# Performance work log

Hardware: AMD Instinct MI355X
Metric: run time of the kernel (lower is better)

## Reference

```python
import jax, jax.numpy as jnp
import numpy as np

# SLAYER SRM-alpha neuron constants (from network.yaml defaults)
THETA = 10.0      # spike threshold
TAU_S = 10.0      # PSP (srm) time constant
TAU_R = 1.0       # refractory time constant
TS = 1.0          # simulation timestep
TAU_RHO = 1.0     # surrogate gradient width
SCALE_RHO = 1.0   # surrogate gradient scale
E = float(np.e)

@jax.custom_vjp
def spike_fn(v):
    # Heaviside threshold; surrogate gradient in bwd (SLAYER spike pdf)
    return (v >= 0).astype(v.dtype)

def _spike_fwd(v):
    return spike_fn(v), v

def _spike_bwd(v, g):
    sg = (SCALE_RHO / TAU_RHO) * jnp.exp(-jnp.abs(v) / TAU_RHO)
    return (g * sg,)

spike_fn.defvjp(_spike_fwd, _spike_bwd)

def psp_spike(a):
    """SLAYER psp (alpha SRM kernel eps(t)=(t/tau_s)e^{1-t/tau_s}, IIR form)
    followed by spike generation with refractory feedback
    nu(t) = -2*theta*(t/tau_r)e^{1-t/tau_r}. a: [B,C,T] -> spikes [B,C,T].
    Alpha kernels realized exactly as 2-state linear recursions."""
    ds = jnp.exp(jnp.asarray(-TS / TAU_S, a.dtype))
    dr = jnp.exp(jnp.asarray(-TS / TAU_R, a.dtype))
    cs = E / TAU_S
    cr = -2.0 * THETA * E / TAU_R
    B, C, T = a.shape
    z = jnp.zeros((B, C), a.dtype)

    def step(carry, a_t):
        xs, ys, xr, yr = carry
        u = cs * ys + cr * yr          # membrane = psp(a) + refractory
        s = spike_fn(u - THETA)
        xs = ds * xs + a_t             # first-order stage (input)
        ys = ds * (ys + TS * xs)       # alpha stage: ys[t+1]=d*(ys+Ts*xs)
        xr = dr * xr + s               # refractory stages driven by spikes
        yr = dr * (yr + TS * xr)
        return (xs, ys, xr, yr), s

    _, s = jax.lax.scan(step, (z, z, z, z), jnp.moveaxis(a, -1, 0))
    return jnp.moveaxis(s, 0, -1)

def psp(a):
    """Pure SLAYER psp filter (no spiking). a: [B,C,T] -> [B,C,T]."""
    ds = jnp.exp(jnp.asarray(-TS / TAU_S, a.dtype))
    cs = E / TAU_S
    B, C, T = a.shape
    z = jnp.zeros((B, C), a.dtype)

    def step(carry, a_t):
        xs, ys = carry
        p = cs * ys
        xs = ds * xs + a_t
        ys = ds * (ys + TS * xs)
        return (xs, ys), p

    _, p = jax.lax.scan(step, (z, z), jnp.moveaxis(a, -1, 0))
    return jnp.moveaxis(p, 0, -1)

def setup_inputs() -> dict:
    key = jax.random.key(0)
    k1, k2, k3 = jax.random.split(key, 3)
    B, NIN, H, NOUT, T = 64, 4, 512, 2, 2000
    # sparse binary input spike trains, rate ~0.1
    spikeInput = (jax.random.uniform(k1, (B, NIN, T)) < 0.1).astype(jnp.float32)
    W1 = 2.0 * jax.random.normal(k2, (H, NIN), jnp.float32)
    W2 = 2.0 * jax.random.normal(k3, (NOUT, H), jnp.float32)
    return {"spikeInput": spikeInput, "W1": W1, "W2": W2}

def reference(spikeInput, W1, W2):
    # fc1 -> psp -> spike
    s1 = psp_spike(jnp.einsum('oi,bit->bot', W1, spikeInput))
    # fc2 -> psp -> spike
    s2 = psp_spike(jnp.einsum('oh,bht->bot', W2, s1))
    # final psp readout
    return psp(s2)
```

## Files before the change

kernel.cpp:

```cpp
#include <hip/hip_runtime.h>
#include <cstdint>
#include <cstddef>

#define THETA_F 10.0f
#define DS_C 0.9048374180359595731642491f
#define DR_C 0.3678794411714423215955238f
#define CS_C 0.2718281828459045235360287f
#define CR_C -54.3656365691809047072057f
#define P100_C 4.5399929762484854e-05f
#define QC100_C 4.1079555325e-03f

typedef unsigned int       u32;
typedef unsigned long long u64;
typedef unsigned short     u16;

#define W32_WORDS_PER_B  (62 * 512)
#define TAIL_BYTE_OFF    (64 * 62 * 512 * 4)

__global__ __launch_bounds__(128) void k1_layer1(
    const float* __restrict__ inp,
    const float* __restrict__ W1,
    u32* __restrict__ w32, u16* __restrict__ tail16)
{
    __shared__ float table[16 * 128];
    __shared__ alignas(8) unsigned char codes[2048];

    const int tid = threadIdx.x;
    const int b   = blockIdx.x >> 2;
    const int h   = ((blockIdx.x & 3) << 7) + tid;

    const float w0 = W1[h * 4 + 0];
    const float w1 = W1[h * 4 + 1];
    const float w2 = W1[h * 4 + 2];
    const float w3 = W1[h * 4 + 3];
    for (int c = 0; c < 16; ++c) {
        float v = __fmul_rn(w0, (c & 1) ? 1.0f : 0.0f);
        v = __fadd_rn(v, __fmul_rn(w1, (c & 2) ? 1.0f : 0.0f));
        v = __fadd_rn(v, __fmul_rn(w2, (c & 4) ? 1.0f : 0.0f));
        v = __fadd_rn(v, __fmul_rn(w3, (c & 8) ? 1.0f : 0.0f));
        table[c * 128 + tid] = v;
    }
    for (int t = tid; t < 2000; t += 128) {
        const float v0 = inp[(b * 4 + 0) * 2000 + t];
        const float v1 = inp[(b * 4 + 1) * 2000 + t];
        const float v2 = inp[(b * 4 + 2) * 2000 + t];
        const float v3 = inp[(b * 4 + 3) * 2000 + t];
        codes[t] = (unsigned char)((int)(v0 != 0.0f) | ((int)(v1 != 0.0f) << 1) |
                                   ((int)(v2 != 0.0f) << 2) | ((int)(v3 != 0.0f) << 3));
    }
    if (tid < 48) codes[2000 + tid] = 0;
    __syncthreads();

#define ISSUE(CW, BUF) do {                                                   \
        const u32 lo_ = (u32)(CW), hi_ = (u32)((CW) >> 32);                   \
        BUF[0] = table[((lo_      ) & 15) * 128 + tid];                       \
        BUF[1] = table[((lo_ >>  8) & 15) * 128 + tid];                       \
        BUF[2] = table[((lo_ >> 16) & 15) * 128 + tid];                       \
        BUF[3] = table[((lo_ >> 24) & 15) * 128 + tid];                       \
        BUF[4] = table[((hi_      ) & 15) * 128 + tid];                       \
        BUF[5] = table[((hi_ >>  8) & 15) * 128 + tid];                       \
        BUF[6] = table[((hi_ >> 16) & 15) * 128 + tid];                       \
        BUF[7] = table[((hi_ >> 24) & 15) * 128 + tid];                       \
    } while (0)

#define STEP(AV, BITPOS) do {                                                 \
        const float u_ = __fadd_rn(__fmul_rn(CS_C, ys), __fmul_rn(CR_C, yr)); \
        const bool sp_ = (u_ >= THETA_F);                                     \
        xs = __fadd_rn(__fmul_rn(DS_C, xs), (AV));                            \
        ys = __fmul_rn(DS_C, __fadd_rn(ys, xs));                              \
        const float A_ = __fmul_rn(DR_C, xr);                                 \
        xr = sp_ ? __fadd_rn(A_, 1.0f) : A_;                                  \
        yr = __fmul_rn(DR_C, __fadd_rn(yr, xr));                              \
        bits = sp_ ? (bits | (1u << (BITPOS))) : bits;                        \
    } while (0)

#define STEP8(BUF, J0) do {                                                   \
        _Pragma("unroll")                                                     \
        for (int j_ = 0; j_ < 8; ++j_) STEP(BUF[j_], (J0) + j_);              \
    } while (0)

    float xs = 0.0f, ys = 0.0f, xr = 0.0f, yr = 0.0f;
    u32 bits = 0;
    u32* pw = w32 + (size_t)b * W32_WORDS_PER_B + h;

    float bA[8], bB[8];
    u64 cw = *reinterpret_cast<const u64*>(codes);
    ISSUE(cw, bA);
    u64 c1 = *reinterpret_cast<const u64*>(codes + 8);
    u64 c2 = *reinterpret_cast<const u64*>(codes + 16);
    u64 c3 = *reinterpret_cast<const u64*>(codes + 24);
    u64 c4 = *reinterpret_cast<const u64*>(codes + 32);

    for (int t0 = 0; t0 < 1984; t0 += 32) {
        ISSUE(c1, bB);
        const u64 n1 = *reinterpret_cast<const u64*>(codes + t0 + 40);
        const u64 n2 = *reinterpret_cast<const u64*>(codes + t0 + 48);
        const u64 n3 = *reinterpret_cast<const u64*>(codes + t0 + 56);
        const u64 n4 = *reinterpret_cast<const u64*>(codes + t0 + 64);
        STEP8(bA, 0);
        ISSUE(c2, bA);
        STEP8(bB, 8);
        ISSUE(c3, bB);
        STEP8(bA, 16);
        ISSUE(c4, bA);
        STEP8(bB, 24);
        *pw = bits; pw += 512; bits = 0;
        c1 = n1; c2 = n2; c3 = n3; c4 = n4;
    }
    ISSUE(c1, bB);
    STEP8(bA, 0);
    STEP8(bB, 8);
    tail16[b * 512 + h] = (u16)bits;

#undef STEP8
#undef STEP
#undef ISSUE
}

__global__ __launch_bounds__(256) void k2_fc2(
    const u32* __restrict__ w32, const u16* __restrict__ tail16,
    const float* __restrict__ W2,
    float* __restrict__ a2)
{
    __shared__ float w2s[1024];
    __shared__ u32 stage[4096];

    const int tid = threadIdx.x;
    const int b  = blockIdx.x >> 3;
    const int it = blockIdx.x & 7;

    for (int j = tid; j < 1024; j += 256) w2s[j] = W2[j];
    #pragma unroll
    for (int k = 0; k < 16; ++k) {
        const int l = tid + (k << 8);
        const int gtb = (it << 3) + (l >> 9);
        u32 v = 0;
        if (gtb < 62)       v = w32[((size_t)b * 62 + gtb) * 512 + (l & 511)];
        else if (gtb == 62) v = (u32)tail16[b * 512 + (l & 511)];
        stage[l] = v;
    }
    __syncthreads();

    const int t = (it << 8) + tid;
    if (t < 2000) {
        const u32* srow = stage + ((tid >> 5) << 9);
        const int sh = tid & 31;
        float acc0 = 0.0f, acc1 = 0.0f;
        #pragma unroll 8
        for (int hh = 0; hh < 512; ++hh) {
            const bool on = (srow[hh] >> sh) & 1u;
            acc0 = __fadd_rn(acc0, on ? w2s[hh] : 0.0f);
            acc1 = __fadd_rn(acc1, on ? w2s[512 + hh] : 0.0f);
        }
        a2[(size_t)(b * 2 + 0) * 2000 + t] = acc0;
        a2[(size_t)(b * 2 + 1) * 2000 + t] = acc1;
    }
}

__global__ __launch_bounds__(80) void k3all(
    const float* __restrict__ a2, float* __restrict__ out)
{
    __shared__ float U[4][2000];
    __shared__ unsigned char s2b[4][2000];
    __shared__ float ex[4][20], ey[4][20], px[4][20], py[4][20];

    const int tid = threadIdx.x;
    const int lc  = tid / 20;
    const int ck  = tid - lc * 20;
    const int chain = blockIdx.x * 4 + lc;

    {
        const float* segi = a2 + (size_t)chain * 2000 + ck * 100;
        float* segU = &U[lc][ck * 100];
        float X = 0.0f, Y = 0.0f;
        for (int g = 0; g < 25; ++g) {
            float4 qv = *reinterpret_cast<const float4*>(segi + 4 * g);
            float z;
            z = __fmul_rn(CS_C, Y); X = __fmaf_rn(DS_C, X, qv.x);
            Y = __fmul_rn(DS_C, __fadd_rn(Y, X)); qv.x = z;
            z = __fmul_rn(CS_C, Y); X = __fmaf_rn(DS_C, X, qv.y);
            Y = __fmul_rn(DS_C, __fadd_rn(Y, X)); qv.y = z;
            z = __fmul_rn(CS_C, Y); X = __fmaf_rn(DS_C, X, qv.z);
            Y = __fmul_rn(DS_C, __fadd_rn(Y, X)); qv.z = z;
            z = __fmul_rn(CS_C, Y); X = __fmaf_rn(DS_C, X, qv.w);
            Y = __fmul_rn(DS_C, __fadd_rn(Y, X)); qv.w = z;
            *reinterpret_cast<float4*>(segU + 4 * g) = qv;
        }
        ex[lc][ck] = X; ey[lc][ck] = Y;
    }
    __syncthreads();
    if (tid < 4) {
        float x = 0.0f, y = 0.0f;
        for (int c = 0; c < 20; ++c) {
            px[tid][c] = x; py[tid][c] = y;
            const float xn = __fmaf_rn(P100_C, x, ex[tid][c]);
            const float yn = __fadd_rn(
                __fmaf_rn(QC100_C, x, __fmul_rn(P100_C, y)), ey[tid][c]);
            x = xn; y = yn;
        }
    }
    __syncthreads();
    {
        float xh = px[lc][ck], yh = py[lc][ck];
        float* segU = &U[lc][ck * 100];
        if (ck != 0) {
            for (int g = 0; g < 25; ++g) {
                float4 qv = *reinterpret_cast<const float4*>(segU + 4 * g);
                qv.x = __fmaf_rn(CS_C, yh, qv.x);
                xh = __fmul_rn(DS_C, xh); yh = __fmul_rn(DS_C, __fadd_rn(yh, xh));
                qv.y = __fmaf_rn(CS_C, yh, qv.y);
                xh = __fmul_rn(DS_C, xh); yh = __fmul_rn(DS_C, __fadd_rn(yh, xh));
                qv.z = __fmaf_rn(CS_C, yh, qv.z);
                xh = __fmul_rn(DS_C, xh); yh = __fmul_rn(DS_C, __fadd_rn(yh, xh));
                qv.w = __fmaf_rn(CS_C, yh, qv.w);
                xh = __fmul_rn(DS_C, xh); yh = __fmul_rn(DS_C, __fadd_rn(yh, xh));
                *reinterpret_cast<float4*>(segU + 4 * g) = qv;
            }
        }
    }
    __syncthreads();

    {
        float xr2 = 0.0f, yr2 = 0.0f;
#define RSTEP(UV) do {                                                        \
        const float u_ = __fadd_rn((UV), __fmul_rn(CR_C, yr2));               \
        const bool sp_ = (u_ >= THETA_F);                                     \
        const float A_ = __fmul_rn(DR_C, xr2);                                \
        xr2 = sp_ ? __fadd_rn(A_, 1.0f) : A_;                                 \
        yr2 = __fmul_rn(DR_C, __fadd_rn(yr2, xr2));                           \
    } while (0)
        if (ck != 0) {
            const float* wseg = &U[lc][ck * 100 - 64];
            #pragma unroll
            for (int g = 0; g < 16; ++g) {
                const float4 qv = *reinterpret_cast<const float4*>(wseg + 4 * g);
                RSTEP(qv.x); RSTEP(qv.y); RSTEP(qv.z); RSTEP(qv.w);
            }
        }
        const float* eseg = &U[lc][ck * 100];
        unsigned char* ob = &s2b[lc][ck * 100];
        for (int g = 0; g < 25; ++g) {
            const float4 qv = *reinterpret_cast<const float4*>(eseg + 4 * g);
            const float uv[4] = {qv.x, qv.y, qv.z, qv.w};
            #pragma unroll
            for (int j = 0; j < 4; ++j) {
                const float u_ = __fadd_rn(uv[j], __fmul_rn(CR_C, yr2));
                const bool sp_ = (u_ >= THETA_F);
                ob[4 * g + j] = sp_ ? 1 : 0;
                const float A_ = __fmul_rn(DR_C, xr2);
                xr2 = sp_ ? __fadd_rn(A_, 1.0f) : A_;
                yr2 = __fmul_rn(DR_C, __fadd_rn(yr2, xr2));
            }
        }
#undef RSTEP
    }
    __syncthreads();

    float* sego = out + (size_t)chain * 2000 + ck * 100;
    {
        const unsigned char* si = &s2b[lc][ck * 100];
        float X = 0.0f, Y = 0.0f;
        for (int j = 0; j < 100; ++j) {
            const float a = (float)si[j];
            const float z = __fmul_rn(CS_C, Y);
            X = __fmaf_rn(DS_C, X, a);
            Y = __fmul_rn(DS_C, __fadd_rn(Y, X));
            sego[j] = z;
        }
        ex[lc][ck] = X; ey[lc][ck] = Y;
    }
    __syncthreads();
    if (tid < 4) {
        float x = 0.0f, y = 0.0f;
        for (int c = 0; c < 20; ++c) {
            px[tid][c] = x; py[tid][c] = y;
            const float xn = __fmaf_rn(P100_C, x, ex[tid][c]);
            const float yn = __fadd_rn(
                __fmaf_rn(QC100_C, x, __fmul_rn(P100_C, y)), ey[tid][c]);
            x = xn; y = yn;
        }
    }
    __syncthreads();
    {
        float xh = px[lc][ck], yh = py[lc][ck];
        if (ck != 0) {
            for (int j = 0; j < 100; ++j) {
                sego[j] = __fmaf_rn(CS_C, yh, sego[j]);
                xh = __fmul_rn(DS_C, xh);
                yh = __fmul_rn(DS_C, __fadd_rn(yh, xh));
            }
        }
    }
}

extern "C" void kernel_launch(void* const* d_in, const int* in_sizes, int n_in,
                              void* d_out, int out_size, void* d_ws, size_t ws_size,
                              hipStream_t stream)
{
    const float* inp = (const float*)d_in[0];
    const float* W1  = (const float*)d_in[1];
    const float* W2  = (const float*)d_in[2];
    float* out = (float*)d_out;

    u32* w32    = (u32*)d_ws;
    u16* tail16 = (u16*)((char*)d_ws + TAIL_BYTE_OFF);

    k1_layer1<<<dim3(256), dim3(128), 0, stream>>>(inp, W1, w32, tail16);
    k2_fc2<<<dim3(512), dim3(256), 0, stream>>>(w32, tail16, W2, out);
    k3all<<<dim3(32), dim3(80), 0, stream>>>(out, out);
}
```

Before: 137.5 us.

## Run two independent neuron recurrences per thread in layer-1 kernel

Each thread of the layer-1 scan kernel now advances two hidden neurons (h and h+256) at once, with one 64-thread wave per block instead of 128 threads. Interleaving two independent serial recurrences gives more instruction-level parallelism to hide the dependent FMA latency of the scan, and shares the code-word decode across both neurons. The cost is half as many waves in flight per block and more register pressure.

```diff
diff --git a/kernel.cpp b/kernel.cpp
--- a/kernel.cpp
+++ b/kernel.cpp
@@ -17,30 +17,39 @@
 #define W32_WORDS_PER_B  (62 * 512)
 #define TAIL_BYTE_OFF    (64 * 62 * 512 * 4)
 
-__global__ __launch_bounds__(128) void k1_layer1(
+__global__ __launch_bounds__(64) void k1_dual(
     const float* __restrict__ inp,
     const float* __restrict__ W1,
     u32* __restrict__ w32, u16* __restrict__ tail16)
 {
-    __shared__ float table[16 * 128];
+    __shared__ float table[32 * 64];
     __shared__ alignas(8) unsigned char codes[2048];
 
     const int tid = threadIdx.x;
     const int b   = blockIdx.x >> 2;
-    const int h   = ((blockIdx.x & 3) << 7) + tid;
-
-    const float w0 = W1[h * 4 + 0];
-    const float w1 = W1[h * 4 + 1];
-    const float w2 = W1[h * 4 + 2];
-    const float w3 = W1[h * 4 + 3];
-    for (int c = 0; c < 16; ++c) {
-        float v = __fmul_rn(w0, (c & 1) ? 1.0f : 0.0f);
-        v = __fadd_rn(v, __fmul_rn(w1, (c & 2) ? 1.0f : 0.0f));
-        v = __fadd_rn(v, __fmul_rn(w2, (c & 4) ? 1.0f : 0.0f));
-        v = __fadd_rn(v, __fmul_rn(w3, (c & 8) ? 1.0f : 0.0f));
-        table[c * 128 + tid] = v;
-    }
-    for (int t = tid; t < 2000; t += 128) {
+    const int q   = blockIdx.x & 3;
+    const int h1  = (q << 6) + tid;
+    const int h2  = h1 + 256;
+
+    {
+        const float a0 = W1[h1 * 4 + 0], a1 = W1[h1 * 4 + 1];
+        const float a2 = W1[h1 * 4 + 2], a3 = W1[h1 * 4 + 3];
+        const float b0 = W1[h2 * 4 + 0], b1 = W1[h2 * 4 + 1];
+        const float b2 = W1[h2 * 4 + 2], b3 = W1[h2 * 4 + 3];
+        for (int c = 0; c < 16; ++c) {
+            float v = __fmul_rn(a0, (c & 1) ? 1.0f : 0.0f);
+            v = __fadd_rn(v, __fmul_rn(a1, (c & 2) ? 1.0f : 0.0f));
+            v = __fadd_rn(v, __fmul_rn(a2, (c & 4) ? 1.0f : 0.0f));
+            v = __fadd_rn(v, __fmul_rn(a3, (c & 8) ? 1.0f : 0.0f));
+            table[c * 64 + tid] = v;
+            float w = __fmul_rn(b0, (c & 1) ? 1.0f : 0.0f);
+            w = __fadd_rn(w, __fmul_rn(b1, (c & 2) ? 1.0f : 0.0f));
+            w = __fadd_rn(w, __fmul_rn(b2, (c & 4) ? 1.0f : 0.0f));
+            w = __fadd_rn(w, __fmul_rn(b3, (c & 8) ? 1.0f : 0.0f));
+            table[(c + 16) * 64 + tid] = w;
+        }
+    }
+    for (int t = tid; t < 2000; t += 64) {
         const float v0 = inp[(b * 4 + 0) * 2000 + t];
         const float v1 = inp[(b * 4 + 1) * 2000 + t];
         const float v2 = inp[(b * 4 + 2) * 2000 + t];
@@ -51,70 +60,83 @@
     if (tid < 48) codes[2000 + tid] = 0;
     __syncthreads();
 
-#define ISSUE(CW, BUF) do {                                                   \
+#define ISSUE2(CW, B1, B2) do {                                               \
         const u32 lo_ = (u32)(CW), hi_ = (u32)((CW) >> 32);                   \
-        BUF[0] = table[((lo_      ) & 15) * 128 + tid];                       \
-        BUF[1] = table[((lo_ >>  8) & 15) * 128 + tid];                       \
-        BUF[2] = table[((lo_ >> 16) & 15) * 128 + tid];                       \
-        BUF[3] = table[((lo_ >> 24) & 15) * 128 + tid];                       \
-        BUF[4] = table[((hi_      ) & 15) * 128 + tid];                       \
-        BUF[5] = table[((hi_ >>  8) & 15) * 128 + tid];                       \
-        BUF[6] = table[((hi_ >> 16) & 15) * 128 + tid];                       \
-        BUF[7] = table[((hi_ >> 24) & 15) * 128 + tid];                       \
+        _Pragma("unroll")                                                     \
+        for (int j_ = 0; j_ < 4; ++j_) {                                      \
+            const float* p_ = &table[(int)((lo_ >> (8 * j_)) & 15) * 64 + tid]; \
+            B1[j_] = p_[0];  B2[j_] = p_[1024];                               \
+        }                                                                     \
+        _Pragma("unroll")                                                     \
+        for (int j_ = 0; j_ < 4; ++j_) {                                      \
+            const float* p_ = &table[(int)((hi_ >> (8 * j_)) & 15) * 64 + tid]; \
+            B1[4 + j_] = p_[0];  B2[4 + j_] = p_[1024];                       \
+        }                                                                     \
     } while (0)
 
-#define STEP(AV, BITPOS) do {                                                 \
-        const float u_ = __fadd_rn(__fmul_rn(CS_C, ys), __fmul_rn(CR_C, yr)); \
-        const bool sp_ = (u_ >= THETA_F);                                     \
-        xs = __fadd_rn(__fmul_rn(DS_C, xs), (AV));                            \
-        ys = __fmul_rn(DS_C, __fadd_rn(ys, xs));                              \
-        const float A_ = __fmul_rn(DR_C, xr);                                 \
-        xr = sp_ ? __fadd_rn(A_, 1.0f) : A_;                                  \
-        yr = __fmul_rn(DR_C, __fadd_rn(yr, xr));                              \
-        bits = sp_ ? (bits | (1u << (BITPOS))) : bits;                        \
+#define STEP2(A1, A2, BITPOS) do {                                            \
+        const float u1_ = __fadd_rn(__fmul_rn(CS_C, ys1), __fmul_rn(CR_C, yr1)); \
+        const float u2_ = __fadd_rn(__fmul_rn(CS_C, ys2), __fmul_rn(CR_C, yr2)); \
+        const bool s1_ = (u1_ >= THETA_F);                                    \
+        const bool s2_ = (u2_ >= THETA_F);                                    \
+        xs1 = __fadd_rn(__fmul_rn(DS_C, xs1), (A1));                          \
+        xs2 = __fadd_rn(__fmul_rn(DS_C, xs2), (A2));                          \
+        ys1 = __fmul_rn(DS_C, __fadd_rn(ys1, xs1));                           \
+        ys2 = __fmul_rn(DS_C, __fadd_rn(ys2, xs2));                           \
+        const float A1_ = __fmul_rn(DR_C, xr1);                               \
+        const float A2_ = __fmul_rn(DR_C, xr2);                               \
+        xr1 = s1_ ? __fadd_rn(A1_, 1.0f) : A1_;                               \
+        xr2 = s2_ ? __fadd_rn(A2_, 1.0f) : A2_;                               \
+        yr1 = __fmul_rn(DR_C, __fadd_rn(yr1, xr1));                           \
+        yr2 = __fmul_rn(DR_C, __fadd_rn(yr2, xr2));                           \
+        bits1 = s1_ ? (bits1 | (1u << (BITPOS))) : bits1;                     \
+        bits2 = s2_ ? (bits2 | (1u << (BITPOS))) : bits2;                     \
     } while (0)
 
-#define STEP8(BUF, J0) do {                                                   \
+#define STEP8x2(B1, B2, J0) do {                                              \
         _Pragma("unroll")                                                     \
-        for (int j_ = 0; j_ < 8; ++j_) STEP(BUF[j_], (J0) + j_);              \
+        for (int j_ = 0; j_ < 8; ++j_) STEP2(B1[j_], B2[j_], (J0) + j_);      \
     } while (0)
 
-    float xs = 0.0f, ys = 0.0f, xr = 0.0f, yr = 0.0f;
-    u32 bits = 0;
-    u32* pw = w32 + (size_t)b * W32_WORDS_PER_B + h;
-
-    float bA[8], bB[8];
+    float xs1 = 0.0f, ys1 = 0.0f, xr1 = 0.0f, yr1 = 0.0f;
+    float xs2 = 0.0f, ys2 = 0.0f, xr2 = 0.0f, yr2 = 0.0f;
+    u32 bits1 = 0, bits2 = 0;
+    u32* pw = w32 + (size_t)b * W32_WORDS_PER_B + h1;
+
+    float bA1[8], bA2[8], bB1[8], bB2[8];
     u64 cw = *reinterpret_cast<const u64*>(codes);
-    ISSUE(cw, bA);
+    ISSUE2(cw, bA1, bA2);
     u64 c1 = *reinterpret_cast<const u64*>(codes + 8);
     u64 c2 = *reinterpret_cast<const u64*>(codes + 16);
     u64 c3 = *reinterpret_cast<const u64*>(codes + 24);
     u64 c4 = *reinterpret_cast<const u64*>(codes + 32);
 
     for (int t0 = 0; t0 < 1984; t0 += 32) {
-        ISSUE(c1, bB);
+        ISSUE2(c1, bB1, bB2);
         const u64 n1 = *reinterpret_cast<const u64*>(codes + t0 + 40);
         const u64 n2 = *reinterpret_cast<const u64*>(codes + t0 + 48);
         const u64 n3 = *reinterpret_cast<const u64*>(codes + t0 + 56);
         const u64 n4 = *reinterpret_cast<const u64*>(codes + t0 + 64);
-        STEP8(bA, 0);
-        ISSUE(c2, bA);
-        STEP8(bB, 8);
-        ISSUE(c3, bB);
-        STEP8(bA, 16);
-        ISSUE(c4, bA);
-        STEP8(bB, 24);
-        *pw = bits; pw += 512; bits = 0;
+        STEP8x2(bA1, bA2, 0);
+        ISSUE2(c2, bA1, bA2);
+        STEP8x2(bB1, bB2, 8);
+        ISSUE2(c3, bB1, bB2);
+        STEP8x2(bA1, bA2, 16);
+        ISSUE2(c4, bA1, bA2);
+        STEP8x2(bB1, bB2, 24);
+        pw[0] = bits1; pw[256] = bits2;
+        pw += 512; bits1 = 0; bits2 = 0;
         c1 = n1; c2 = n2; c3 = n3; c4 = n4;
     }
-    ISSUE(c1, bB);
-    STEP8(bA, 0);
-    STEP8(bB, 8);
-    tail16[b * 512 + h] = (u16)bits;
-
-#undef STEP8
-#undef STEP
-#undef ISSUE
+    ISSUE2(c1, bB1, bB2);
+    STEP8x2(bA1, bA2, 0);
+    STEP8x2(bB1, bB2, 8);
+    tail16[b * 512 + h1] = (u16)bits1;
+    tail16[b * 512 + h2] = (u16)bits2;
+
+#undef STEP8x2
+#undef STEP2
+#undef ISSUE2
 }
 
 __global__ __launch_bounds__(256) void k2_fc2(
@@ -305,7 +327,7 @@
     u32* w32    = (u32*)d_ws;
     u16* tail16 = (u16*)((char*)d_ws + TAIL_BYTE_OFF);
 
-    k1_layer1<<<dim3(256), dim3(128), 0, stream>>>(inp, W1, w32, tail16);
+    k1_dual<<<dim3(256), dim3(64), 0, stream>>>(inp, W1, w32, tail16);
     k2_fc2<<<dim3(512), dim3(256), 0, stream>>>(w32, tail16, W2, out);
     k3all<<<dim3(32), dim3(80), 0, stream>>>(out, out);
 }
```

Result: slower. 150.1 us (+9.1%).
